# Kernel optimization log

Measured on AMD Instinct MI355X. Metric: run time of the kernel, lower is better.

Reference implementation:

```python
import jax, jax.numpy as jnp
import numpy as np

KS = 3                       # unfold kernel size
DILATIONS = (1, 3)           # LAE dilation branches
HEAD_DIM = 32                # dim // num_heads = 256 // 8
SCALE_DILATE = HEAD_DIM ** -0.5
SCALE_GAE = 0.177            # round(32**-0.5, 3) as in ESFF.__init__
WS = 2                       # GAE avg-pool window
L_HEADS = 4                  # int(8 * 0.5)
L_DIM = 128                  # l_heads * head_dim


def _unfold3(x, d):
    """nn.Unfold(kernel=3, dilation=d, padding=d, stride=1) without the flatten.
    x: [B, C, H, W] -> [B, C, 9, H, W] (kernel positions in (kh, kw) row-major order,
    matching torch's channel-major unfold layout)."""
    B, C, H, W = x.shape
    xp = jnp.pad(x, ((0, 0), (0, 0), (d, d), (d, d)))
    patches = [xp[:, :, i * d:i * d + H, j * d:j * d + W]
               for i in range(KS) for j in range(KS)]
    return jnp.stack(patches, axis=2)


def _dilate_attention(q, k, v, dil):
    """q,k,v: [B, d, H, W] -> [B, H, W, d]. Per-pixel 1x9 attention over dilated 3x3 window."""
    B, d, H, W = q.shape
    nh = d // HEAD_DIM
    qr = q.reshape(B, nh, HEAD_DIM, H * W)                      # [B,nh,hd,P]
    kp = _unfold3(k, dil).reshape(B, nh, HEAD_DIM, KS * KS, H * W)
    attn = jnp.einsum('bncp,bncjp->bnpj', qr, kp) * SCALE_DILATE  # [B,nh,P,9]
    attn = jax.nn.softmax(attn, axis=-1)
    vp = _unfold3(v, dil).reshape(B, nh, HEAD_DIM, KS * KS, H * W)
    out = jnp.einsum('bnpj,bncjp->bnpc', attn, vp)              # [B,nh,P,hd]
    return out.transpose(0, 2, 1, 3).reshape(B, H, W, d)


def _lae(x, qkv_w, proj_w, proj_b):
    """LAE_Attention. x: [B,H,W,C]. Note: torch detaches qkv, so this branch
    carries no gradient; we mirror that with stop_gradient."""
    B, H, W, C = x.shape
    nd = len(DILATIONS)
    qkv = jnp.einsum('bhwc,oc->bhwo', x, qkv_w)                 # 1x1 conv, [B,H,W,3C]
    qkv = jax.lax.stop_gradient(qkv)
    qkv = qkv.transpose(0, 3, 1, 2).reshape(B, 3, nd, C // nd, H, W)
    qkv = qkv.transpose(2, 1, 0, 3, 4, 5)                       # [nd,3,B,C/nd,H,W]
    outs = [_dilate_attention(qkv[i, 0], qkv[i, 1], qkv[i, 2], DILATIONS[i])
            for i in range(nd)]                                  # each [B,H,W,C/nd]
    y = jnp.stack(outs, axis=0).transpose(1, 2, 3, 0, 4).reshape(B, H, W, C)
    return y @ proj_w.T + proj_b


def _gae(x, lq_w, lkv_w, lproj_w, lproj_b):
    """GAE_Attention: full-res queries attend to 2x2 avg-pooled KV."""
    B, H, W, C = x.shape
    hd = HEAD_DIM
    q = (x.reshape(B, H * W, C) @ lq_w.T)
    q = q.reshape(B, H * W, L_HEADS, hd).transpose(0, 2, 1, 3)   # [B,lh,HW,hd]
    xs = x.reshape(B, H // WS, WS, W // WS, WS, C).mean(axis=(2, 4))  # avg pool -> [B,7,7,C]
    kv = (xs.reshape(B, -1, C) @ lkv_w.T)
    kv = kv.reshape(B, -1, 2, L_HEADS, hd).transpose(2, 0, 3, 1, 4)   # [2,B,lh,49,hd]
    k, v = kv[0], kv[1]
    attn = jax.nn.softmax(jnp.einsum('bhqd,bhkd->bhqk', q, k) * SCALE_GAE, axis=-1)
    out = jnp.einsum('bhqk,bhkd->bhqd', attn, v)
    out = out.transpose(0, 2, 1, 3).reshape(B, H, W, L_DIM)
    return out @ lproj_w.T + lproj_b


def setup_inputs() -> dict:
    key = jax.random.key(0)
    ks = jax.random.split(key, 10)
    dim = 256
    f = lambda k, shape, scale: (jax.random.normal(k, shape, dtype=jnp.float32) * scale)
    return {
        'x': f(ks[0], (28, 14, 14, dim), 1.0),
        'qkv_w': f(ks[1], (3 * dim, dim), dim ** -0.5),      # 1x1 conv weight
        'lae_proj_w': f(ks[2], (dim, dim), dim ** -0.5),
        'lae_proj_b': jnp.zeros((dim,), jnp.float32),
        'lq_w': f(ks[3], (L_DIM, dim), dim ** -0.5),
        'lkv_w': f(ks[4], (2 * L_DIM, dim), dim ** -0.5),
        'lproj_w': f(ks[5], (L_DIM, L_DIM), L_DIM ** -0.5),
        'lproj_b': jnp.zeros((L_DIM,), jnp.float32),
        'cls_w': f(ks[6], (2, 75264), 75264 ** -0.5),
        'cls_b': jnp.zeros((2,), jnp.float32),
    }


def reference(x, qkv_w, lae_proj_w, lae_proj_b, lq_w, lkv_w, lproj_w, lproj_b, cls_w, cls_b):
    B, H, W, C = x.shape                                    # [28,14,14,256]
    x = x.reshape(4, 7, H, W, C).mean(axis=1)               # [4,14,14,256]
    lae_out = _lae(x, qkv_w, lae_proj_w, lae_proj_b)        # [4,14,14,256]
    gae_out = _gae(x, lq_w, lkv_w, lproj_w, lproj_b)        # [4,14,14,128]
    y = jnp.concatenate([lae_out, gae_out], axis=-1)        # [4,14,14,384]
    y = y.reshape(4, H * W * (C + L_DIM))                   # [4,75264]
    return y @ cls_w.T + cls_b                              # [4,2]
```

## Files before the change

### kernel.cpp

```cpp
#include <hip/hip_runtime.h>


#define WS_XM    0
#define WS_XS    200704
#define WS_QKV   250880
#define WS_QB    852992
#define WS_KVB   953344
#define WS_Y     1003520
#define WS_GA    1204224

__global__ __launch_bounds__(256) void k_mean_pool(const float* __restrict__ x,
                                                   const float* __restrict__ cls_b,
                                                   float* __restrict__ xm,
                                                   float* __restrict__ xs,
                                                   float* __restrict__ out) {
  const int blk = blockIdx.x;
  const int b = blk / 49;
  const int q = blk % 49;
  const int ph2 = q / 7, pw2 = q % 7;
  const int c = threadIdx.x;
  float s4 = 0.f;
  #pragma unroll
  for (int dy = 0; dy < 2; ++dy) {
    #pragma unroll
    for (int dx = 0; dx < 2; ++dx) {
      const int p = (ph2 * 2 + dy) * 14 + (pw2 * 2 + dx);
      float s = 0.f;
      #pragma unroll
      for (int g = 0; g < 7; ++g)
        s += x[((b * 7 + g) * 196 + p) * 256 + c];
      s *= (1.f / 7.f);
      xm[(b * 196 + p) * 256 + c] = s;
      s4 += s;
    }
  }
  xs[(b * 49 + q) * 256 + c] = s4 * 0.25f;
  if (blk == 0 && c < 8) out[c] = cls_b[c & 1];
}

__global__ __launch_bounds__(256) void k_proj_in(const float* __restrict__ xm,
                                                 const float* __restrict__ xs,
                                                 const float* __restrict__ qkv_w,
                                                 const float* __restrict__ lq_w,
                                                 const float* __restrict__ lkv_w,
                                                 float* __restrict__ qkvb,
                                                 float* __restrict__ qb,
                                                 float* __restrict__ kvb) {
  __shared__ float As[32][68];
  __shared__ float Bs[64][68];
  const int tid = threadIdx.x;
  const int tx = tid & 15, ty = tid >> 4;
  const int bid = blockIdx.x;
  int region, mt, nt;
  if (bid < 350) { region = 0; mt = bid / 14; nt = bid % 14; }
  else { const int r = bid - 350; region = 1; mt = r / 4; nt = r % 4; }
  const float* A = region ? xs : xm;
  const int M = region ? 196 : 784;
  const int rowBase = mt * 32;
  const int colBase = nt * 64;

  float acc[2][4] = {{0.f,0.f,0.f,0.f},{0.f,0.f,0.f,0.f}};

  for (int kc = 0; kc < 256; kc += 64) {
    #pragma unroll
    for (int i = 0; i < 2; ++i) {
      const int e = tid + i * 256;
      const int r = e >> 4, k4 = (e & 15) << 2;
      const int row = rowBase + r;
      float4 v = make_float4(0.f, 0.f, 0.f, 0.f);
      if (row < M) v = *(const float4*)(A + (size_t)row * 256 + kc + k4);
      *(float4*)(&As[r][k4]) = v;
    }
    #pragma unroll
    for (int i = 0; i < 4; ++i) {
      const int e = tid + i * 256;
      const int n = e >> 4, k4 = (e & 15) << 2;
      const int col = colBase + n;
      const float* Wp; int wr;
      if (region == 1)      { Wp = lkv_w; wr = col; }
      else if (col < 768)   { Wp = qkv_w; wr = col; }
      else                  { Wp = lq_w;  wr = col - 768; }
      *(float4*)(&Bs[n][k4]) = *(const float4*)(Wp + (size_t)wr * 256 + kc + k4);
    }
    __syncthreads();
    #pragma unroll
    for (int k = 0; k < 64; k += 4) {
      const float4 a0 = *(const float4*)(&As[ty][k]);
      const float4 a1 = *(const float4*)(&As[ty + 16][k]);
      const float4 c0 = *(const float4*)(&Bs[tx][k]);
      const float4 c1 = *(const float4*)(&Bs[tx + 16][k]);
      const float4 c2 = *(const float4*)(&Bs[tx + 32][k]);
      const float4 c3 = *(const float4*)(&Bs[tx + 48][k]);
      acc[0][0] += a0.x*c0.x + a0.y*c0.y + a0.z*c0.z + a0.w*c0.w;
      acc[0][1] += a0.x*c1.x + a0.y*c1.y + a0.z*c1.z + a0.w*c1.w;
      acc[0][2] += a0.x*c2.x + a0.y*c2.y + a0.z*c2.z + a0.w*c2.w;
      acc[0][3] += a0.x*c3.x + a0.y*c3.y + a0.z*c3.z + a0.w*c3.w;
      acc[1][0] += a1.x*c0.x + a1.y*c0.y + a1.z*c0.z + a1.w*c0.w;
      acc[1][1] += a1.x*c1.x + a1.y*c1.y + a1.z*c1.z + a1.w*c1.w;
      acc[1][2] += a1.x*c2.x + a1.y*c2.y + a1.z*c2.z + a1.w*c2.w;
      acc[1][3] += a1.x*c3.x + a1.y*c3.y + a1.z*c3.z + a1.w*c3.w;
    }
    __syncthreads();
  }

  #pragma unroll
  for (int j = 0; j < 4; ++j) {
    const int col = colBase + tx + 16 * j;
    #pragma unroll
    for (int i = 0; i < 2; ++i) {
      const int row = rowBase + ty + 16 * i;
      if (row >= M) continue;
      if (region == 1)    kvb[(size_t)row * 256 + col] = acc[i][j];
      else if (col < 768) qkvb[(size_t)row * 768 + col] = acc[i][j];
      else                qb[(size_t)row * 128 + col - 768] = acc[i][j];
    }
  }
}

__global__ __launch_bounds__(256) void k_attn(const float* __restrict__ qkvb,
                                              const float* __restrict__ qb,
                                              const float* __restrict__ kvb,
                                              float* __restrict__ y,
                                              float* __restrict__ ga) {
  __shared__ float Ks[49][32];
  __shared__ float Vs[49][32];
  const int bid = blockIdx.x;
  const int tid = threadIdx.x;

  if (bid < 784) {
    const int b = bid / 196, p = bid % 196;
    const int ph = p / 14, pw = p % 14;
    const int c = tid;
    const int d = (c < 128) ? 1 : 3;
    const float qv = qkvb[(size_t)bid * 768 + c];
    float s[9];
    #pragma unroll
    for (int j = 0; j < 9; ++j) {
      const int nh = ph + (j / 3 - 1) * d;
      const int nw = pw + (j % 3 - 1) * d;
      float kval = 0.f;
      if ((unsigned)nh < 14u && (unsigned)nw < 14u)
        kval = qkvb[((size_t)(b * 196 + nh * 14 + nw)) * 768 + 256 + c];
      float t = qv * kval;
      t += __shfl_xor(t, 1);
      t += __shfl_xor(t, 2);
      t += __shfl_xor(t, 4);
      t += __shfl_xor(t, 8);
      t += __shfl_xor(t, 16);
      s[j] = t * 0.17677669529663687f;
    }
    float mx = s[0];
    #pragma unroll
    for (int j = 1; j < 9; ++j) mx = fmaxf(mx, s[j]);
    float sum = 0.f;
    #pragma unroll
    for (int j = 0; j < 9; ++j) { s[j] = __expf(s[j] - mx); sum += s[j]; }
    const float inv = 1.f / sum;
    float o = 0.f;
    #pragma unroll
    for (int j = 0; j < 9; ++j) {
      const int nh = ph + (j / 3 - 1) * d;
      const int nw = pw + (j % 3 - 1) * d;
      if ((unsigned)nh < 14u && (unsigned)nw < 14u)
        o += s[j] * qkvb[((size_t)(b * 196 + nh * 14 + nw)) * 768 + 512 + c];
    }
    y[(size_t)bid * 256 + c] = o * inv;
  } else {
    const int g = bid - 784;
    const int b = g >> 2, h = g & 3;
    for (int e = tid; e < 49 * 32; e += 256) {
      const int kk = e >> 5, cc = e & 31;
      Ks[kk][cc] = kvb[(size_t)(b * 49 + kk) * 256 + h * 32 + cc];
      Vs[kk][cc] = kvb[(size_t)(b * 49 + kk) * 256 + 128 + h * 32 + cc];
    }
    __syncthreads();
    if (tid < 196) {
      float q[32], o[32];
      #pragma unroll
      for (int cc = 0; cc < 32; ++cc) {
        q[cc] = qb[(size_t)(b * 196 + tid) * 128 + h * 32 + cc];
        o[cc] = 0.f;
      }
      float m = -1e30f, l = 0.f;
      for (int kk = 0; kk < 49; ++kk) {
        float sc = 0.f;
        #pragma unroll
        for (int cc = 0; cc < 32; ++cc) sc += q[cc] * Ks[kk][cc];
        sc *= 0.177f;
        if (sc > m) {
          const float r = __expf(m - sc);
          l *= r;
          #pragma unroll
          for (int cc = 0; cc < 32; ++cc) o[cc] *= r;
          m = sc;
        }
        const float pch = __expf(sc - m);
        l += pch;
        #pragma unroll
        for (int cc = 0; cc < 32; ++cc) o[cc] += pch * Vs[kk][cc];
      }
      const float inv = 1.f / l;
      #pragma unroll
      for (int cc = 0; cc < 32; ++cc)
        ga[(size_t)(b * 196 + tid) * 128 + h * 32 + cc] = o[cc] * inv;
    }
  }
}

__global__ __launch_bounds__(256) void k_proj_cls(const float* __restrict__ y,
                                                  const float* __restrict__ ga,
                                                  const float* __restrict__ lae_w,
                                                  const float* __restrict__ lae_b,
                                                  const float* __restrict__ lproj_w,
                                                  const float* __restrict__ lproj_b,
                                                  const float* __restrict__ cw,
                                                  float* __restrict__ out) {
  __shared__ float As[32][68];
  __shared__ float Bs[64][68];
  const int tid = threadIdx.x;
  const int tx = tid & 15, ty = tid >> 4;
  const int bid = blockIdx.x;
  int region, b, pt, nt;
  if (bid < 112) { region = 0; b = bid / 28; const int r = bid % 28; pt = r / 4; nt = r % 4; }
  else { const int q = bid - 112; region = 1; b = q / 14; const int r = q % 14; pt = r / 2; nt = r % 2; }

  const float* A; const float* W; const float* bias;
  int lda, K, colOff;
  if (region == 0) { A = y  + (size_t)b * 196 * 256; lda = 256; K = 256; W = lae_w;   bias = lae_b;   colOff = 0; }
  else             { A = ga + (size_t)b * 196 * 128; lda = 128; K = 128; W = lproj_w; bias = lproj_b; colOff = 256; }
  const int colBase = nt * 64;

  float acc[2][4] = {{0.f,0.f,0.f,0.f},{0.f,0.f,0.f,0.f}};

  for (int kc = 0; kc < K; kc += 64) {
    #pragma unroll
    for (int i = 0; i < 2; ++i) {
      const int e = tid + i * 256;
      const int r = e >> 4, k4 = (e & 15) << 2;
      const int p = pt * 32 + r;
      float4 v = make_float4(0.f, 0.f, 0.f, 0.f);
      if (p < 196) v = *(const float4*)(A + (size_t)p * lda + kc + k4);
      *(float4*)(&As[r][k4]) = v;
    }
    #pragma unroll
    for (int i = 0; i < 4; ++i) {
      const int e = tid + i * 256;
      const int n = e >> 4, k4 = (e & 15) << 2;
      const int col = colBase + n;
      *(float4*)(&Bs[n][k4]) = *(const float4*)(W + (size_t)col * K + kc + k4);
    }
    __syncthreads();
    #pragma unroll
    for (int k = 0; k < 64; k += 4) {
      const float4 a0 = *(const float4*)(&As[ty][k]);
      const float4 a1 = *(const float4*)(&As[ty + 16][k]);
      const float4 c0 = *(const float4*)(&Bs[tx][k]);
      const float4 c1 = *(const float4*)(&Bs[tx + 16][k]);
      const float4 c2 = *(const float4*)(&Bs[tx + 32][k]);
      const float4 c3 = *(const float4*)(&Bs[tx + 48][k]);
      acc[0][0] += a0.x*c0.x + a0.y*c0.y + a0.z*c0.z + a0.w*c0.w;
      acc[0][1] += a0.x*c1.x + a0.y*c1.y + a0.z*c1.z + a0.w*c1.w;
      acc[0][2] += a0.x*c2.x + a0.y*c2.y + a0.z*c2.z + a0.w*c2.w;
      acc[0][3] += a0.x*c3.x + a0.y*c3.y + a0.z*c3.z + a0.w*c3.w;
      acc[1][0] += a1.x*c0.x + a1.y*c0.y + a1.z*c0.z + a1.w*c0.w;
      acc[1][1] += a1.x*c1.x + a1.y*c1.y + a1.z*c1.z + a1.w*c1.w;
      acc[1][2] += a1.x*c2.x + a1.y*c2.y + a1.z*c2.z + a1.w*c2.w;
      acc[1][3] += a1.x*c3.x + a1.y*c3.y + a1.z*c3.z + a1.w*c3.w;
    }
    __syncthreads();
  }

  float s0 = 0.f, s1 = 0.f;
  #pragma unroll
  for (int j = 0; j < 4; ++j) {
    const int col = colBase + tx + 16 * j;
    const float bv = bias[col];
    #pragma unroll
    for (int i = 0; i < 2; ++i) {
      const int p = pt * 32 + ty + 16 * i;
      if (p >= 196) continue;
      const float v = acc[i][j] + bv;
      const size_t fidx = (size_t)p * 384 + colOff + col;
      s0 += v * cw[fidx];
      s1 += v * cw[75264 + fidx];
    }
  }
  float* red = &As[0][0];
  red[tid] = s0;
  red[256 + tid] = s1;
  __syncthreads();
  for (int st = 128; st > 0; st >>= 1) {
    if (tid < st) { red[tid] += red[tid + st]; red[256 + tid] += red[256 + tid + st]; }
    __syncthreads();
  }
  if (tid == 0) {
    atomicAdd(&out[b * 2 + 0], red[0]);
    atomicAdd(&out[b * 2 + 1], red[256]);
  }
}

extern "C" void kernel_launch(void* const* d_in, const int* in_sizes, int n_in,
                              void* d_out, int out_size, void* d_ws, size_t ws_size,
                              hipStream_t stream) {
  (void)in_sizes; (void)n_in; (void)out_size; (void)ws_size;
  const float* x          = (const float*)d_in[0];
  const float* qkv_w      = (const float*)d_in[1];
  const float* lae_proj_w = (const float*)d_in[2];
  const float* lae_proj_b = (const float*)d_in[3];
  const float* lq_w       = (const float*)d_in[4];
  const float* lkv_w      = (const float*)d_in[5];
  const float* lproj_w    = (const float*)d_in[6];
  const float* lproj_b    = (const float*)d_in[7];
  const float* cls_w      = (const float*)d_in[8];
  const float* cls_b      = (const float*)d_in[9];
  float* out = (float*)d_out;
  float* ws  = (float*)d_ws;

  float* xm   = ws + WS_XM;
  float* xs   = ws + WS_XS;
  float* qkvb = ws + WS_QKV;
  float* qb   = ws + WS_QB;
  float* kvb  = ws + WS_KVB;
  float* y    = ws + WS_Y;
  float* ga   = ws + WS_GA;

  k_mean_pool<<<196, 256, 0, stream>>>(x, cls_b, xm, xs, out);
  k_proj_in<<<378, 256, 0, stream>>>(xm, xs, qkv_w, lq_w, lkv_w, qkvb, qb, kvb);
  k_attn<<<800, 256, 0, stream>>>(qkvb, qb, kvb, y, ga);
  k_proj_cls<<<168, 256, 0, stream>>>(y, ga, lae_proj_w, lae_proj_b,
                                      lproj_w, lproj_b, cls_w, out);
}
```

Before: 130.8 us.

## Fuse four phase kernels into one cooperative persistent kernel with grid syncs

Result: slower. 283.0 us (+116.4%).

```diff
diff --git a/kernel.cpp b/kernel.cpp
--- a/kernel.cpp
+++ b/kernel.cpp
@@ -1,5 +1,10 @@
 #include <hip/hip_runtime.h>
-
+#include <hip/hip_cooperative_groups.h>
+
+namespace cg = cooperative_groups;
+
+
+#define GRID 400
 
 #define WS_XM    0
 #define WS_XS    200704
@@ -9,16 +14,16 @@
 #define WS_Y     1003520
 #define WS_GA    1204224
 
-__global__ __launch_bounds__(256) void k_mean_pool(const float* __restrict__ x,
-                                                   const float* __restrict__ cls_b,
-                                                   float* __restrict__ xm,
-                                                   float* __restrict__ xs,
-                                                   float* __restrict__ out) {
-  const int blk = blockIdx.x;
-  const int b = blk / 49;
-  const int q = blk % 49;
+#define LDS_FLOATS 6528
+#define AS(r,c) lds[(r)*68+(c)]
+#define BS(r,c) lds[2176+(r)*68+(c)]
+
+__device__ __forceinline__ void phase_mean_pool(int blk, int tid,
+    const float* __restrict__ x, const float* __restrict__ cls_b,
+    float* __restrict__ xm, float* __restrict__ xs, float* __restrict__ out) {
+  const int b = blk / 49, q = blk % 49;
   const int ph2 = q / 7, pw2 = q % 7;
-  const int c = threadIdx.x;
+  const int c = tid;
   float s4 = 0.f;
   #pragma unroll
   for (int dy = 0; dy < 2; ++dy) {
@@ -38,26 +43,18 @@
   if (blk == 0 && c < 8) out[c] = cls_b[c & 1];
 }
 
-__global__ __launch_bounds__(256) void k_proj_in(const float* __restrict__ xm,
-                                                 const float* __restrict__ xs,
-                                                 const float* __restrict__ qkv_w,
-                                                 const float* __restrict__ lq_w,
-                                                 const float* __restrict__ lkv_w,
-                                                 float* __restrict__ qkvb,
-                                                 float* __restrict__ qb,
-                                                 float* __restrict__ kvb) {
-  __shared__ float As[32][68];
-  __shared__ float Bs[64][68];
-  const int tid = threadIdx.x;
+__device__ __forceinline__ void phase_proj_in(int bid, int tid, float* lds,
+    const float* __restrict__ xm, const float* __restrict__ xs,
+    const float* __restrict__ qkv_w, const float* __restrict__ lq_w,
+    const float* __restrict__ lkv_w,
+    float* __restrict__ qkvb, float* __restrict__ qb, float* __restrict__ kvb) {
   const int tx = tid & 15, ty = tid >> 4;
-  const int bid = blockIdx.x;
   int region, mt, nt;
   if (bid < 350) { region = 0; mt = bid / 14; nt = bid % 14; }
   else { const int r = bid - 350; region = 1; mt = r / 4; nt = r % 4; }
   const float* A = region ? xs : xm;
   const int M = region ? 196 : 784;
-  const int rowBase = mt * 32;
-  const int colBase = nt * 64;
+  const int rowBase = mt * 32, colBase = nt * 64;
 
   float acc[2][4] = {{0.f,0.f,0.f,0.f},{0.f,0.f,0.f,0.f}};
 
@@ -69,7 +66,7 @@
       const int row = rowBase + r;
       float4 v = make_float4(0.f, 0.f, 0.f, 0.f);
       if (row < M) v = *(const float4*)(A + (size_t)row * 256 + kc + k4);
-      *(float4*)(&As[r][k4]) = v;
+      *(float4*)(&AS(r, k4)) = v;
     }
     #pragma unroll
     for (int i = 0; i < 4; ++i) {
@@ -80,17 +77,17 @@
       if (region == 1)      { Wp = lkv_w; wr = col; }
       else if (col < 768)   { Wp = qkv_w; wr = col; }
       else                  { Wp = lq_w;  wr = col - 768; }
-      *(float4*)(&Bs[n][k4]) = *(const float4*)(Wp + (size_t)wr * 256 + kc + k4);
+      *(float4*)(&BS(n, k4)) = *(const float4*)(Wp + (size_t)wr * 256 + kc + k4);
     }
     __syncthreads();
     #pragma unroll
     for (int k = 0; k < 64; k += 4) {
-      const float4 a0 = *(const float4*)(&As[ty][k]);
-      const float4 a1 = *(const float4*)(&As[ty + 16][k]);
-      const float4 c0 = *(const float4*)(&Bs[tx][k]);
-      const float4 c1 = *(const float4*)(&Bs[tx + 16][k]);
-      const float4 c2 = *(const float4*)(&Bs[tx + 32][k]);
-      const float4 c3 = *(const float4*)(&Bs[tx + 48][k]);
+      const float4 a0 = *(const float4*)(&AS(ty, k));
+      const float4 a1 = *(const float4*)(&AS(ty + 16, k));
+      const float4 c0 = *(const float4*)(&BS(tx, k));
+      const float4 c1 = *(const float4*)(&BS(tx + 16, k));
+      const float4 c2 = *(const float4*)(&BS(tx + 32, k));
+      const float4 c3 = *(const float4*)(&BS(tx + 48, k));
       acc[0][0] += a0.x*c0.x + a0.y*c0.y + a0.z*c0.z + a0.w*c0.w;
       acc[0][1] += a0.x*c1.x + a0.y*c1.y + a0.z*c1.z + a0.w*c1.w;
       acc[0][2] += a0.x*c2.x + a0.y*c2.y + a0.z*c2.z + a0.w*c2.w;
@@ -117,16 +114,9 @@
   }
 }
 
-__global__ __launch_bounds__(256) void k_attn(const float* __restrict__ qkvb,
-                                              const float* __restrict__ qb,
-                                              const float* __restrict__ kvb,
-                                              float* __restrict__ y,
-                                              float* __restrict__ ga) {
-  __shared__ float Ks[49][32];
-  __shared__ float Vs[49][32];
-  const int bid = blockIdx.x;
-  const int tid = threadIdx.x;
-
+__device__ __forceinline__ void phase_attn(int bid, int tid, float* lds,
+    const float* __restrict__ qkvb, const float* __restrict__ qb,
+    const float* __restrict__ kvb, float* __restrict__ y, float* __restrict__ ga) {
   if (bid < 784) {
     const int b = bid / 196, p = bid % 196;
     const int ph = p / 14, pw = p % 14;
@@ -168,10 +158,12 @@
   } else {
     const int g = bid - 784;
     const int b = g >> 2, h = g & 3;
+    float* Ks = lds;
+    float* Vs = lds + 1568;
     for (int e = tid; e < 49 * 32; e += 256) {
       const int kk = e >> 5, cc = e & 31;
-      Ks[kk][cc] = kvb[(size_t)(b * 49 + kk) * 256 + h * 32 + cc];
-      Vs[kk][cc] = kvb[(size_t)(b * 49 + kk) * 256 + 128 + h * 32 + cc];
+      Ks[e] = kvb[(size_t)(b * 49 + kk) * 256 + h * 32 + cc];
+      Vs[e] = kvb[(size_t)(b * 49 + kk) * 256 + 128 + h * 32 + cc];
     }
     __syncthreads();
     if (tid < 196) {
@@ -185,7 +177,7 @@
       for (int kk = 0; kk < 49; ++kk) {
         float sc = 0.f;
         #pragma unroll
-        for (int cc = 0; cc < 32; ++cc) sc += q[cc] * Ks[kk][cc];
+        for (int cc = 0; cc < 32; ++cc) sc += q[cc] * Ks[kk * 32 + cc];
         sc *= 0.177f;
         if (sc > m) {
           const float r = __expf(m - sc);
@@ -197,29 +189,23 @@
         const float pch = __expf(sc - m);
         l += pch;
         #pragma unroll
-        for (int cc = 0; cc < 32; ++cc) o[cc] += pch * Vs[kk][cc];
+        for (int cc = 0; cc < 32; ++cc) o[cc] += pch * Vs[kk * 32 + cc];
       }
       const float inv = 1.f / l;
       #pragma unroll
       for (int cc = 0; cc < 32; ++cc)
         ga[(size_t)(b * 196 + tid) * 128 + h * 32 + cc] = o[cc] * inv;
     }
-  }
-}
-
-__global__ __launch_bounds__(256) void k_proj_cls(const float* __restrict__ y,
-                                                  const float* __restrict__ ga,
-                                                  const float* __restrict__ lae_w,
-                                                  const float* __restrict__ lae_b,
-                                                  const float* __restrict__ lproj_w,
-                                                  const float* __restrict__ lproj_b,
-                                                  const float* __restrict__ cw,
-                                                  float* __restrict__ out) {
-  __shared__ float As[32][68];
-  __shared__ float Bs[64][68];
-  const int tid = threadIdx.x;
+    __syncthreads();
+  }
+}
+
+__device__ __forceinline__ void phase_proj_cls(int bid, int tid, float* lds,
+    const float* __restrict__ y, const float* __restrict__ ga,
+    const float* __restrict__ lae_w, const float* __restrict__ lae_b,
+    const float* __restrict__ lproj_w, const float* __restrict__ lproj_b,
+    const float* __restrict__ cw, float* __restrict__ out) {
   const int tx = tid & 15, ty = tid >> 4;
-  const int bid = blockIdx.x;
   int region, b, pt, nt;
   if (bid < 112) { region = 0; b = bid / 28; const int r = bid % 28; pt = r / 4; nt = r % 4; }
   else { const int q = bid - 112; region = 1; b = q / 14; const int r = q % 14; pt = r / 2; nt = r % 2; }
@@ -240,24 +226,24 @@
       const int p = pt * 32 + r;
       float4 v = make_float4(0.f, 0.f, 0.f, 0.f);
       if (p < 196) v = *(const float4*)(A + (size_t)p * lda + kc + k4);
-      *(float4*)(&As[r][k4]) = v;
+      *(float4*)(&AS(r, k4)) = v;
     }
     #pragma unroll
     for (int i = 0; i < 4; ++i) {
       const int e = tid + i * 256;
       const int n = e >> 4, k4 = (e & 15) << 2;
       const int col = colBase + n;
-      *(float4*)(&Bs[n][k4]) = *(const float4*)(W + (size_t)col * K + kc + k4);
+      *(float4*)(&BS(n, k4)) = *(const float4*)(W + (size_t)col * K + kc + k4);
     }
     __syncthreads();
     #pragma unroll
     for (int k = 0; k < 64; k += 4) {
-      const float4 a0 = *(const float4*)(&As[ty][k]);
-      const float4 a1 = *(const float4*)(&As[ty + 16][k]);
-      const float4 c0 = *(const float4*)(&Bs[tx][k]);
-      const float4 c1 = *(const float4*)(&Bs[tx + 16][k]);
-      const float4 c2 = *(const float4*)(&Bs[tx + 32][k]);
-      const float4 c3 = *(const float4*)(&Bs[tx + 48][k]);
+      const float4 a0 = *(const float4*)(&AS(ty, k));
+      const float4 a1 = *(const float4*)(&AS(ty + 16, k));
+      const float4 c0 = *(const float4*)(&BS(tx, k));
+      const float4 c1 = *(const float4*)(&BS(tx + 16, k));
+      const float4 c2 = *(const float4*)(&BS(tx + 32, k));
+      const float4 c3 = *(const float4*)(&BS(tx + 48, k));
       acc[0][0] += a0.x*c0.x + a0.y*c0.y + a0.z*c0.z + a0.w*c0.w;
       acc[0][1] += a0.x*c1.x + a0.y*c1.y + a0.z*c1.z + a0.w*c1.w;
       acc[0][2] += a0.x*c2.x + a0.y*c2.y + a0.z*c2.z + a0.w*c2.w;
@@ -285,7 +271,7 @@
       s1 += v * cw[75264 + fidx];
     }
   }
-  float* red = &As[0][0];
+  float* red = lds;
   red[tid] = s0;
   red[256 + tid] = s1;
   __syncthreads();
@@ -297,6 +283,49 @@
     atomicAdd(&out[b * 2 + 0], red[0]);
     atomicAdd(&out[b * 2 + 1], red[256]);
   }
+}
+
+__global__ __launch_bounds__(256, 2) void k_fused(
+    const float* x, const float* qkv_w, const float* lae_w, const float* lae_b,
+    const float* lq_w, const float* lkv_w, const float* lproj_w, const float* lproj_b,
+    const float* cls_w, const float* cls_b, float* out,
+    float* xm, float* xs, float* qkvb, float* qb, float* kvb, float* y, float* ga) {
+  __shared__ float lds[LDS_FLOATS];
+  cg::grid_group grid = cg::this_grid();
+  const int bid = blockIdx.x, tid = threadIdx.x;
+
+  if (bid < 196) phase_mean_pool(bid, tid, x, cls_b, xm, xs, out);
+  grid.sync();
+  if (bid < 378) phase_proj_in(bid, tid, lds, xm, xs, qkv_w, lq_w, lkv_w, qkvb, qb, kvb);
+  grid.sync();
+  phase_attn(bid, tid, lds, qkvb, qb, kvb, y, ga);
+  phase_attn(bid + GRID, tid, lds, qkvb, qb, kvb, y, ga);
+  grid.sync();
+  if (bid < 168) phase_proj_cls(bid, tid, lds, y, ga, lae_w, lae_b, lproj_w, lproj_b, cls_w, out);
+}
+
+__global__ __launch_bounds__(256, 2) void k_p0(const float* x, const float* cls_b,
+                                               float* xm, float* xs, float* out) {
+  phase_mean_pool(blockIdx.x, threadIdx.x, x, cls_b, xm, xs, out);
+}
+__global__ __launch_bounds__(256, 2) void k_p1(const float* xm, const float* xs,
+                                               const float* qkv_w, const float* lq_w,
+                                               const float* lkv_w, float* qkvb,
+                                               float* qb, float* kvb) {
+  __shared__ float lds[LDS_FLOATS];
+  phase_proj_in(blockIdx.x, threadIdx.x, lds, xm, xs, qkv_w, lq_w, lkv_w, qkvb, qb, kvb);
+}
+__global__ __launch_bounds__(256, 2) void k_p2(const float* qkvb, const float* qb,
+                                               const float* kvb, float* y, float* ga) {
+  __shared__ float lds[LDS_FLOATS];
+  phase_attn(blockIdx.x, threadIdx.x, lds, qkvb, qb, kvb, y, ga);
+}
+__global__ __launch_bounds__(256, 2) void k_p3(const float* y, const float* ga,
+                                               const float* lae_w, const float* lae_b,
+                                               const float* lproj_w, const float* lproj_b,
+                                               const float* cw, float* out) {
+  __shared__ float lds[LDS_FLOATS];
+  phase_proj_cls(blockIdx.x, threadIdx.x, lds, y, ga, lae_w, lae_b, lproj_w, lproj_b, cw, out);
 }
 
 extern "C" void kernel_launch(void* const* d_in, const int* in_sizes, int n_in,
@@ -324,9 +353,20 @@
   float* y    = ws + WS_Y;
   float* ga   = ws + WS_GA;
 
-  k_mean_pool<<<196, 256, 0, stream>>>(x, cls_b, xm, xs, out);
-  k_proj_in<<<378, 256, 0, stream>>>(xm, xs, qkv_w, lq_w, lkv_w, qkvb, qb, kvb);
-  k_attn<<<800, 256, 0, stream>>>(qkvb, qb, kvb, y, ga);
-  k_proj_cls<<<168, 256, 0, stream>>>(y, ga, lae_proj_w, lae_proj_b,
-                                      lproj_w, lproj_b, cls_w, out);
-}
+  void* args[18] = {
+    (void*)&x, (void*)&qkv_w, (void*)&lae_proj_w, (void*)&lae_proj_b,
+    (void*)&lq_w, (void*)&lkv_w, (void*)&lproj_w, (void*)&lproj_b,
+    (void*)&cls_w, (void*)&cls_b, (void*)&out,
+    (void*)&xm, (void*)&xs, (void*)&qkvb, (void*)&qb, (void*)&kvb,
+    (void*)&y, (void*)&ga };
+
+  hipError_t err = hipLaunchCooperativeKernel((const void*)k_fused, dim3(GRID),
+                                              dim3(256), args, 0u, stream);
+  if (err != hipSuccess) {
+    k_p0<<<196, 256, 0, stream>>>(x, cls_b, xm, xs, out);
+    k_p1<<<378, 256, 0, stream>>>(xm, xs, qkv_w, lq_w, lkv_w, qkvb, qb, kvb);
+    k_p2<<<800, 256, 0, stream>>>(qkvb, qb, kvb, y, ga);
+    k_p3<<<168, 256, 0, stream>>>(y, ga, lae_proj_w, lae_proj_b,
+                                  lproj_w, lproj_b, cls_w, out);
+  }
+}
```
